# Kernel optimization log

Measured on AMD Instinct MI355X. Metric: run time of the kernel, lower is better.

Reference implementation:

```python
import jax, jax.numpy as jnp
import numpy as np

B, C, H, W = 32, 512, 32, 32
D = C // 8

def setup_inputs() -> dict:
    key = jax.random.key(0)
    ks = jax.random.split(key, 5)
    return {
        "x": jax.random.normal(ks[0], (B, C, H, W), dtype=jnp.float32),
        "w1": jax.random.normal(ks[1], (D, C), dtype=jnp.float32) * (1.0 / np.sqrt(C)),
        "b1": jax.random.normal(ks[2], (D,), dtype=jnp.float32) * 0.01,
        "w2": jax.random.normal(ks[3], (C, C), dtype=jnp.float32) * (1.0 / np.sqrt(C)),
        "b2": jax.random.normal(ks[4], (C,), dtype=jnp.float32) * 0.01,
    }

def reference(x, w1, b1, w2, b2):
    b, c, h, w = x.shape
    n = h * w
    xf = x.reshape(b, c, n)                                   # [B,C,N]
    # 1x1 convs == channel-mixing GEMMs; conv1 is shared for q and k
    qk = jnp.einsum('bcn,dc->bdn', xf, w1) + b1[None, :, None]  # [B,D,N]
    v = jnp.einsum('bcn,oc->bon', xf, w2) + b2[None, :, None]   # [B,C,N]
    q = qk.transpose(0, 2, 1)                                 # [B,N,D]
    attn = jax.nn.softmax(jnp.einsum('bnd,bdm->bnm', q, qk), axis=-1)  # [B,N,N]
    out = jnp.einsum('bnm,bcm->bnc', attn, v)                 # [B,N,C]
    # Faithful quirk: original views [B,N,C] directly as [B,C,H,W] (no transpose)
    return x + out.reshape(b, c, h, w)
```

## Files before the change

### kernel.cpp

```cpp
#include <hip/hip_runtime.h>
#include <hip/hip_bf16.h>
#include <math.h>

#define B_ 32
#define C_ 512
#define N_ 1024
#define D_ 64
#define OPAD 640

typedef __attribute__((ext_vector_type(4))) float f32x4;
typedef __attribute__((ext_vector_type(4))) float float4v;
typedef __attribute__((ext_vector_type(8))) __bf16 bf16x8;

#define MFMA16(a, b, c) __builtin_amdgcn_mfma_f32_16x16x32_bf16((a), (b), (c), 0, 0, 0)

__device__ inline void load_lds16(const void* g, void* l) {
    __builtin_amdgcn_global_load_lds(
        (const __attribute__((address_space(1))) void*)g,
        (__attribute__((address_space(3))) void*)l, 16, 0, 0);
}

__global__ void k_cast_weights(const float* __restrict__ w1,
                               const float* __restrict__ w2,
                               __hip_bfloat16* __restrict__ Wbf) {
    int idx = blockIdx.x * 256 + threadIdx.x;
    if (idx >= OPAD * C_) return;
    int m = idx >> 9;
    int k = idx & (C_ - 1);
    float val = (m < D_) ? w1[m * C_ + k]
              : (m < D_ + C_) ? w2[(m - D_) * C_ + k] : 0.0f;
    Wbf[idx] = __float2bfloat16(val);
}

__global__ __launch_bounds__(256) void k_transpose_cast(
        const float* __restrict__ x, __hip_bfloat16* __restrict__ xT) {
    __shared__ float tile[64][68];
    int b = blockIdx.z;
    int n0 = blockIdx.x * 64;
    int c0 = blockIdx.y * 64;
    int t = threadIdx.x;
    const float* xb = x + (size_t)b * (C_ * N_);
#pragma unroll
    for (int i = 0; i < 4; i++) {
        int c = i * 16 + (t >> 4);
        int nc = (t & 15) * 4;
        *(float4v*)&tile[c][nc] =
            *(const float4v*)(xb + (size_t)(c0 + c) * N_ + n0 + nc);
    }
    __syncthreads();
    __hip_bfloat16* xTb = xT + (size_t)b * (N_ * C_);
#pragma unroll
    for (int i = 0; i < 2; i++) {
        int n = i * 32 + (t >> 3);
        int cs = (t & 7) * 8;
        alignas(16) __hip_bfloat16 tmp[8];
#pragma unroll
        for (int j = 0; j < 8; j++)
            tmp[j] = __float2bfloat16(tile[cs + j][n]);
        *(bf16x8*)(xTb + (size_t)(n0 + n) * C_ + c0 + cs) = *(bf16x8*)tmp;
    }
}

__global__ __launch_bounds__(256) void k_gemm_qkv(
        const __hip_bfloat16* __restrict__ Wbf,
        const __hip_bfloat16* __restrict__ xT,
        const float* __restrict__ b1, const float* __restrict__ b2,
        __hip_bfloat16* __restrict__ qkT, __hip_bfloat16* __restrict__ v) {
    __shared__ __hip_bfloat16 As[128 * 64];
    __shared__ __hip_bfloat16 Bs[128 * 64];
    __shared__ __hip_bfloat16 epi[4][16][72];
    int b = blockIdx.z;
    int t = threadIdx.x;
    int wave = t >> 6, lane = t & 63, lr = lane & 15, quad = lane >> 4;
    int wm = wave >> 1, wn = wave & 1;
    int m_blk = blockIdx.y * 128;
    int n_blk = blockIdx.x * 128;
    const __hip_bfloat16* xTb = xT + (size_t)b * (N_ * C_);

    f32x4 acc[4][4] = {};
    for (int kk = 0; kk < C_; kk += 64) {
#pragma unroll
        for (int i = 0; i < 4; i++) {
            int id = i * 256 + t;
            int r = id >> 3, cx = id & 7;
            int gc = cx ^ (r & 7);
            load_lds16(Wbf + (size_t)(m_blk + r) * C_ + kk + gc * 8, &As[id * 8]);
            load_lds16(xTb + (size_t)(n_blk + r) * C_ + kk + gc * 8, &Bs[id * 8]);
        }
        __syncthreads();
#pragma unroll
        for (int h = 0; h < 2; h++) {
            bf16x8 af[4], bfr[4];
#pragma unroll
            for (int i = 0; i < 4; i++) {
                int ra = wm * 64 + i * 16 + lr;
                int rb = wn * 64 + i * 16 + lr;
                int q = h * 4 + quad;
                af[i]  = *(const bf16x8*)&As[ra * 64 + (q ^ (lr & 7)) * 8];
                bfr[i] = *(const bf16x8*)&Bs[rb * 64 + (q ^ (lr & 7)) * 8];
            }
#pragma unroll
            for (int mt = 0; mt < 4; mt++)
#pragma unroll
                for (int nt = 0; nt < 4; nt++)
                    acc[mt][nt] = MFMA16(af[mt], bfr[nt], acc[mt][nt]);
        }
        __syncthreads();
    }

#pragma unroll
    for (int mt = 0; mt < 4; mt++) {
        int m_frag = m_blk + wm * 64 + mt * 16;
        if (m_frag >= D_ + C_) continue;
        int m0 = m_frag + quad * 4;
        if (m_frag < D_) {
#pragma unroll
            for (int nt = 0; nt < 4; nt++) {
                int n = n_blk + wn * 64 + nt * 16 + lr;
                alignas(8) __hip_bfloat16 tmp[4];
#pragma unroll
                for (int r = 0; r < 4; r++)
                    tmp[r] = __float2bfloat16(acc[mt][nt][r] + b1[m0 + r]);
                *reinterpret_cast<short4*>(qkT + ((size_t)b * N_ + n) * D_ + m0) =
                    *reinterpret_cast<short4*>(tmp);
            }
        } else {
#pragma unroll
            for (int nt = 0; nt < 4; nt++) {
#pragma unroll
                for (int r = 0; r < 4; r++) {
                    int c = m0 - D_ + r;
                    epi[wave][quad * 4 + r][nt * 16 + lr] =
                        __float2bfloat16(acc[mt][nt][r] + b2[c]);
                }
            }
            int cbase = m_frag - D_;
            int row = lane >> 2;
#pragma unroll
            for (int it = 0; it < 2; it++) {
                int col = it * 32 + (lane & 3) * 8;
                bf16x8 frag = *(const bf16x8*)&epi[wave][row][col];
                *(bf16x8*)(v + (size_t)(b * C_ + cbase + row) * N_
                             + n_blk + wn * 64 + col) = frag;
            }
        }
    }
}

__global__ __launch_bounds__(256) void k_softmax_p(
        const __hip_bfloat16* __restrict__ qkT,
        float* __restrict__ rowinv, __hip_bfloat16* __restrict__ P) {
    __shared__ __hip_bfloat16 Ks[128][72];
    __shared__ __hip_bfloat16 pbuf[4][16][136];
    int b = blockIdx.y;
    int t = threadIdx.x;
    int wave = t >> 6, lane = t & 63, lr = lane & 15, quad = lane >> 4;
    int q0 = blockIdx.x * 64 + wave * 16;
    const __hip_bfloat16* qb = qkT + (size_t)b * (N_ * D_);
    __hip_bfloat16* Pb = P + ((size_t)b << 20);

    bf16x8 a0 = *(const bf16x8*)(qb + (size_t)(q0 + lr) * D_ + quad * 8);
    bf16x8 a1 = *(const bf16x8*)(qb + (size_t)(q0 + lr) * D_ + 32 + quad * 8);

    float mr[4];
#pragma unroll
    for (int r = 0; r < 4; r++) mr[r] = -INFINITY;

    for (int mc = 0; mc < N_; mc += 128) {
#pragma unroll
        for (int i = 0; i < 4; i++) {
            int row = i * 32 + (t >> 3);
            int col = (t & 7) * 8;
            *(bf16x8*)&Ks[row][col] =
                *(const bf16x8*)(qb + (size_t)(mc + row) * D_ + col);
        }
        __syncthreads();
#pragma unroll
        for (int sub = 0; sub < 8; sub++) {
            bf16x8 k0 = *(const bf16x8*)&Ks[sub * 16 + lr][quad * 8];
            bf16x8 k1 = *(const bf16x8*)&Ks[sub * 16 + lr][32 + quad * 8];
            f32x4 s = {};
            s = MFMA16(a0, k0, s);
            s = MFMA16(a1, k1, s);
#pragma unroll
            for (int r = 0; r < 4; r++) mr[r] = fmaxf(mr[r], s[r]);
        }
        __syncthreads();
    }
#pragma unroll
    for (int off = 1; off < 16; off <<= 1)
#pragma unroll
        for (int r = 0; r < 4; r++)
            mr[r] = fmaxf(mr[r], __shfl_xor(mr[r], off));

    float sr[4] = {0.f, 0.f, 0.f, 0.f};
    for (int mc = 0; mc < N_; mc += 128) {
#pragma unroll
        for (int i = 0; i < 4; i++) {
            int row = i * 32 + (t >> 3);
            int col = (t & 7) * 8;
            *(bf16x8*)&Ks[row][col] =
                *(const bf16x8*)(qb + (size_t)(mc + row) * D_ + col);
        }
        __syncthreads();
#pragma unroll
        for (int sub = 0; sub < 8; sub++) {
            bf16x8 k0 = *(const bf16x8*)&Ks[sub * 16 + lr][quad * 8];
            bf16x8 k1 = *(const bf16x8*)&Ks[sub * 16 + lr][32 + quad * 8];
            f32x4 s = {};
            s = MFMA16(a0, k0, s);
            s = MFMA16(a1, k1, s);
#pragma unroll
            for (int r = 0; r < 4; r++) {
                float e = __expf(s[r] - mr[r]);
                sr[r] += e;
                pbuf[wave][quad * 4 + r][sub * 16 + lr] = __float2bfloat16(e);
            }
        }
        int row = lane >> 2;
#pragma unroll
        for (int it = 0; it < 4; it++) {
            int col = it * 32 + (lane & 3) * 8;
            bf16x8 frag = *(const bf16x8*)&pbuf[wave][row][col];
            *(bf16x8*)(Pb + (size_t)(q0 + row) * N_ + mc + col) = frag;
        }
        __syncthreads();
    }
#pragma unroll
    for (int off = 1; off < 16; off <<= 1)
#pragma unroll
        for (int r = 0; r < 4; r++)
            sr[r] += __shfl_xor(sr[r], off);
    if (lr == 0) {
#pragma unroll
        for (int r = 0; r < 4; r++)
            rowinv[b * N_ + q0 + quad * 4 + r] = 1.0f / sr[r];
    }
}

__global__ __launch_bounds__(256) void k_pv_gemm(
        const __hip_bfloat16* __restrict__ P,
        const __hip_bfloat16* __restrict__ v,
        const float* __restrict__ rowinv,
        const float* __restrict__ x, float* __restrict__ out) {
    __shared__ char smem[128 * 64 * 2 * 2];
    __hip_bfloat16* As = (__hip_bfloat16*)smem;
    __hip_bfloat16* Bs = As + 128 * 64;
    float* Obuf = (float*)smem;
    int b = blockIdx.z;
    int t = threadIdx.x;
    int wave = t >> 6, lane = t & 63, lr = lane & 15, quad = lane >> 4;
    int wm = wave >> 1, wn = wave & 1;
    int n_blk = blockIdx.y * 128;
    int c_blk = blockIdx.x * 128;
    const __hip_bfloat16* Pb = P + ((size_t)b << 20);
    const __hip_bfloat16* vb = v + (size_t)b * (C_ * N_);

    f32x4 acc[4][4] = {};
    for (int kk = 0; kk < N_; kk += 64) {
#pragma unroll
        for (int i = 0; i < 4; i++) {
            int id = i * 256 + t;
            int r = id >> 3, cx = id & 7;
            int gc = cx ^ (r & 7);
            load_lds16(Pb + (size_t)(n_blk + r) * N_ + kk + gc * 8, &As[id * 8]);
            load_lds16(vb + (size_t)(c_blk + r) * N_ + kk + gc * 8, &Bs[id * 8]);
        }
        __syncthreads();
#pragma unroll
        for (int h = 0; h < 2; h++) {
            bf16x8 af[4], bfr[4];
#pragma unroll
            for (int i = 0; i < 4; i++) {
                int ra = wm * 64 + i * 16 + lr;
                int rb = wn * 64 + i * 16 + lr;
                int q = h * 4 + quad;
                af[i]  = *(const bf16x8*)&As[ra * 64 + (q ^ (lr & 7)) * 8];
                bfr[i] = *(const bf16x8*)&Bs[rb * 64 + (q ^ (lr & 7)) * 8];
            }
#pragma unroll
            for (int mt = 0; mt < 4; mt++)
#pragma unroll
                for (int nt = 0; nt < 4; nt++)
                    acc[mt][nt] = MFMA16(af[mt], bfr[nt], acc[mt][nt]);
        }
        __syncthreads();
    }

    const float* xb = x + (size_t)b * (N_ * C_);
    float* ob = out + (size_t)b * (N_ * C_);
#pragma unroll
    for (int h = 0; h < 2; h++) {
        if (wm == h) {
#pragma unroll
            for (int mt = 0; mt < 4; mt++)
#pragma unroll
                for (int nt = 0; nt < 4; nt++)
#pragma unroll
                    for (int r = 0; r < 4; r++)
                        Obuf[(mt * 16 + quad * 4 + r) * 128 + wn * 64 + nt * 16 + lr] =
                            acc[mt][nt][r];
        }
        __syncthreads();
#pragma unroll
        for (int i = 0; i < 8; i++) {
            int id = i * 256 + t;
            int rl = id >> 5;
            int c4 = (id & 31) * 4;
            int n = n_blk + h * 64 + rl;
            float ri = rowinv[b * N_ + n];
            float4v o = *(const float4v*)&Obuf[rl * 128 + c4];
            size_t gidx = (size_t)n * C_ + c_blk + c4;
            float4v xv = *(const float4v*)(xb + gidx);
            float4v res;
            res.x = xv.x + ri * o.x;
            res.y = xv.y + ri * o.y;
            res.z = xv.z + ri * o.z;
            res.w = xv.w + ri * o.w;
            *(float4v*)(ob + gidx) = res;
        }
        __syncthreads();
    }
}

extern "C" void kernel_launch(void* const* d_in, const int* in_sizes, int n_in,
                              void* d_out, int out_size, void* d_ws, size_t ws_size,
                              hipStream_t stream) {
    const float* x  = (const float*)d_in[0];
    const float* w1 = (const float*)d_in[1];
    const float* b1 = (const float*)d_in[2];
    const float* w2 = (const float*)d_in[3];
    const float* b2 = (const float*)d_in[4];
    float* out = (float*)d_out;

    char* ws = (char*)d_ws;
    size_t off = 0;
    __hip_bfloat16* Wbf = (__hip_bfloat16*)(ws + off); off += (size_t)OPAD * C_ * 2;
    __hip_bfloat16* xT  = (__hip_bfloat16*)(ws + off); off += (size_t)B_ * N_ * C_ * 2;
    __hip_bfloat16* qkT = (__hip_bfloat16*)(ws + off); off += (size_t)B_ * N_ * D_ * 2;
    __hip_bfloat16* v   = (__hip_bfloat16*)(ws + off); off += (size_t)B_ * C_ * N_ * 2;
    float* rowinv = (float*)(ws + off); off += (size_t)B_ * N_ * 4;
    __hip_bfloat16* P = (__hip_bfloat16*)(ws + off); off += (size_t)B_ * N_ * N_ * 2;

    hipLaunchKernelGGL(k_cast_weights, dim3((OPAD * C_ + 255) / 256), dim3(256), 0, stream,
                       w1, w2, Wbf);
    hipLaunchKernelGGL(k_transpose_cast, dim3(N_ / 64, C_ / 64, B_), dim3(256), 0, stream,
                       x, xT);
    hipLaunchKernelGGL(k_gemm_qkv, dim3(N_ / 128, OPAD / 128, B_), dim3(256), 0, stream,
                       Wbf, xT, b1, b2, qkT, v);
    hipLaunchKernelGGL(k_softmax_p, dim3(N_ / 64, B_), dim3(256), 0, stream,
                       qkT, rowinv, P);
    hipLaunchKernelGGL(k_pv_gemm, dim3(C_ / 128, N_ / 128, B_), dim3(256), 0, stream,
                       P, v, rowinv, x, out);
}
```

Before: 245.2 us.

## Fuse softmax and PV GEMM using per-row norm shift instead of a max pass

Replaces the separate softmax kernel, which wrote a full bf16 P matrix, and the PV GEMM with one fused kernel. Each block recomputes its 128-row slice of QK^T on the fly for every 64-wide key chunk, exponentiates it into LDS and feeds it straight into the PV MFMAs. The row-sum reciprocal is kept in LDS instead of a global buffer. The row-max pass is dropped: the shift is the row's own squared norm ||q_n||^2, which is not a guaranteed upper bound on q·k. That risks overflow for some inputs. It also repeats the QK^T and exp work once per channel block.

```diff
diff --git a/kernel.cpp b/kernel.cpp
--- a/kernel.cpp
+++ b/kernel.cpp
@@ -147,126 +147,96 @@
     }
 }
 
-__global__ __launch_bounds__(256) void k_softmax_p(
+__global__ __launch_bounds__(256) void k_fused_attn(
         const __hip_bfloat16* __restrict__ qkT,
-        float* __restrict__ rowinv, __hip_bfloat16* __restrict__ P) {
-    __shared__ __hip_bfloat16 Ks[128][72];
-    __shared__ __hip_bfloat16 pbuf[4][16][136];
-    int b = blockIdx.y;
-    int t = threadIdx.x;
-    int wave = t >> 6, lane = t & 63, lr = lane & 15, quad = lane >> 4;
-    int q0 = blockIdx.x * 64 + wave * 16;
-    const __hip_bfloat16* qb = qkT + (size_t)b * (N_ * D_);
-    __hip_bfloat16* Pb = P + ((size_t)b << 20);
-
-    bf16x8 a0 = *(const bf16x8*)(qb + (size_t)(q0 + lr) * D_ + quad * 8);
-    bf16x8 a1 = *(const bf16x8*)(qb + (size_t)(q0 + lr) * D_ + 32 + quad * 8);
-
-    float mr[4];
-#pragma unroll
-    for (int r = 0; r < 4; r++) mr[r] = -INFINITY;
-
-    for (int mc = 0; mc < N_; mc += 128) {
-#pragma unroll
-        for (int i = 0; i < 4; i++) {
-            int row = i * 32 + (t >> 3);
-            int col = (t & 7) * 8;
-            *(bf16x8*)&Ks[row][col] =
-                *(const bf16x8*)(qb + (size_t)(mc + row) * D_ + col);
-        }
-        __syncthreads();
-#pragma unroll
-        for (int sub = 0; sub < 8; sub++) {
-            bf16x8 k0 = *(const bf16x8*)&Ks[sub * 16 + lr][quad * 8];
-            bf16x8 k1 = *(const bf16x8*)&Ks[sub * 16 + lr][32 + quad * 8];
-            f32x4 s = {};
-            s = MFMA16(a0, k0, s);
-            s = MFMA16(a1, k1, s);
-#pragma unroll
-            for (int r = 0; r < 4; r++) mr[r] = fmaxf(mr[r], s[r]);
-        }
-        __syncthreads();
-    }
-#pragma unroll
-    for (int off = 1; off < 16; off <<= 1)
-#pragma unroll
-        for (int r = 0; r < 4; r++)
-            mr[r] = fmaxf(mr[r], __shfl_xor(mr[r], off));
-
-    float sr[4] = {0.f, 0.f, 0.f, 0.f};
-    for (int mc = 0; mc < N_; mc += 128) {
-#pragma unroll
-        for (int i = 0; i < 4; i++) {
-            int row = i * 32 + (t >> 3);
-            int col = (t & 7) * 8;
-            *(bf16x8*)&Ks[row][col] =
-                *(const bf16x8*)(qb + (size_t)(mc + row) * D_ + col);
-        }
-        __syncthreads();
-#pragma unroll
-        for (int sub = 0; sub < 8; sub++) {
-            bf16x8 k0 = *(const bf16x8*)&Ks[sub * 16 + lr][quad * 8];
-            bf16x8 k1 = *(const bf16x8*)&Ks[sub * 16 + lr][32 + quad * 8];
-            f32x4 s = {};
-            s = MFMA16(a0, k0, s);
-            s = MFMA16(a1, k1, s);
-#pragma unroll
-            for (int r = 0; r < 4; r++) {
-                float e = __expf(s[r] - mr[r]);
-                sr[r] += e;
-                pbuf[wave][quad * 4 + r][sub * 16 + lr] = __float2bfloat16(e);
-            }
-        }
-        int row = lane >> 2;
-#pragma unroll
-        for (int it = 0; it < 4; it++) {
-            int col = it * 32 + (lane & 3) * 8;
-            bf16x8 frag = *(const bf16x8*)&pbuf[wave][row][col];
-            *(bf16x8*)(Pb + (size_t)(q0 + row) * N_ + mc + col) = frag;
-        }
-        __syncthreads();
-    }
-#pragma unroll
-    for (int off = 1; off < 16; off <<= 1)
-#pragma unroll
-        for (int r = 0; r < 4; r++)
-            sr[r] += __shfl_xor(sr[r], off);
-    if (lr == 0) {
-#pragma unroll
-        for (int r = 0; r < 4; r++)
-            rowinv[b * N_ + q0 + quad * 4 + r] = 1.0f / sr[r];
-    }
-}
-
-__global__ __launch_bounds__(256) void k_pv_gemm(
-        const __hip_bfloat16* __restrict__ P,
         const __hip_bfloat16* __restrict__ v,
-        const float* __restrict__ rowinv,
         const float* __restrict__ x, float* __restrict__ out) {
-    __shared__ char smem[128 * 64 * 2 * 2];
-    __hip_bfloat16* As = (__hip_bfloat16*)smem;
-    __hip_bfloat16* Bs = As + 128 * 64;
+    __shared__ char smem[40960];
+    __hip_bfloat16* Ks = (__hip_bfloat16*)smem;
+    __hip_bfloat16* Vs = (__hip_bfloat16*)(smem + 8192);
+    __hip_bfloat16* Ps = (__hip_bfloat16*)(smem + 24576);
     float* Obuf = (float*)smem;
+    __shared__ float Rs[128];
+
     int b = blockIdx.z;
     int t = threadIdx.x;
     int wave = t >> 6, lane = t & 63, lr = lane & 15, quad = lane >> 4;
     int wm = wave >> 1, wn = wave & 1;
     int n_blk = blockIdx.y * 128;
     int c_blk = blockIdx.x * 128;
-    const __hip_bfloat16* Pb = P + ((size_t)b << 20);
+    const __hip_bfloat16* qb = qkT + (size_t)b * (N_ * D_);
     const __hip_bfloat16* vb = v + (size_t)b * (C_ * N_);
 
+    union bfu { bf16x8 v; __hip_bfloat16 h[8]; };
+    bf16x8 bq[2][2];
+    float shift[2];
+#pragma unroll
+    for (int nj = 0; nj < 2; nj++) {
+        int n = n_blk + wave * 32 + nj * 16 + lr;
+#pragma unroll
+        for (int dh = 0; dh < 2; dh++)
+            bq[nj][dh] = *(const bf16x8*)(qb + (size_t)n * D_ + dh * 32 + quad * 8);
+        float sq = 0.f;
+#pragma unroll
+        for (int dh = 0; dh < 2; dh++) {
+            bfu u; u.v = bq[nj][dh];
+#pragma unroll
+            for (int j = 0; j < 8; j++) {
+                float qv = __bfloat162float(u.h[j]);
+                sq += qv * qv;
+            }
+        }
+        sq += __shfl_xor(sq, 16);
+        sq += __shfl_xor(sq, 32);
+        shift[nj] = sq;
+    }
+
     f32x4 acc[4][4] = {};
+    float rsum[2] = {0.f, 0.f};
+
     for (int kk = 0; kk < N_; kk += 64) {
+#pragma unroll
+        for (int i = 0; i < 2; i++) {
+            int id = i * 256 + t;
+            int r = id >> 3, cx = id & 7;
+            int gc = cx ^ (r & 7);
+            load_lds16(qb + (size_t)(kk + r) * D_ + gc * 8, &Ks[id * 8]);
+        }
 #pragma unroll
         for (int i = 0; i < 4; i++) {
             int id = i * 256 + t;
             int r = id >> 3, cx = id & 7;
             int gc = cx ^ (r & 7);
-            load_lds16(Pb + (size_t)(n_blk + r) * N_ + kk + gc * 8, &As[id * 8]);
-            load_lds16(vb + (size_t)(c_blk + r) * N_ + kk + gc * 8, &Bs[id * 8]);
-        }
-        __syncthreads();
+            load_lds16(vb + (size_t)(c_blk + r) * N_ + kk + gc * 8, &Vs[id * 8]);
+        }
+        __syncthreads();
+
+#pragma unroll
+        for (int mi = 0; mi < 4; mi++) {
+            int m = mi * 16 + lr;
+            bf16x8 ak0 = *(const bf16x8*)&Ks[m * 64 + ((quad) ^ (lr & 7)) * 8];
+            bf16x8 ak1 = *(const bf16x8*)&Ks[m * 64 + ((4 + quad) ^ (lr & 7)) * 8];
+#pragma unroll
+            for (int nj = 0; nj < 2; nj++) {
+                f32x4 s = {};
+                s = MFMA16(ak0, bq[nj][0], s);
+                s = MFMA16(ak1, bq[nj][1], s);
+                alignas(8) __hip_bfloat16 tmp[4];
+#pragma unroll
+                for (int r = 0; r < 4; r++) {
+                    float e = __expf(s[r] - shift[nj]);
+                    rsum[nj] += e;
+                    tmp[r] = __float2bfloat16(e);
+                }
+                int n = wave * 32 + nj * 16 + lr;
+                int cx = mi * 2 + (quad >> 1);
+                int slot = cx ^ (lr & 7);
+                *(short4*)&Ps[n * 64 + slot * 8 + (quad & 1) * 4] =
+                    *(short4*)tmp;
+            }
+        }
+        __syncthreads();
+
 #pragma unroll
         for (int h = 0; h < 2; h++) {
             bf16x8 af[4], bfr[4];
@@ -275,8 +245,8 @@
                 int ra = wm * 64 + i * 16 + lr;
                 int rb = wn * 64 + i * 16 + lr;
                 int q = h * 4 + quad;
-                af[i]  = *(const bf16x8*)&As[ra * 64 + (q ^ (lr & 7)) * 8];
-                bfr[i] = *(const bf16x8*)&Bs[rb * 64 + (q ^ (lr & 7)) * 8];
+                af[i]  = *(const bf16x8*)&Ps[ra * 64 + (q ^ (lr & 7)) * 8];
+                bfr[i] = *(const bf16x8*)&Vs[rb * 64 + (q ^ (lr & 7)) * 8];
             }
 #pragma unroll
             for (int mt = 0; mt < 4; mt++)
@@ -286,6 +256,16 @@
         }
         __syncthreads();
     }
+
+    rsum[0] += __shfl_xor(rsum[0], 16);
+    rsum[0] += __shfl_xor(rsum[0], 32);
+    rsum[1] += __shfl_xor(rsum[1], 16);
+    rsum[1] += __shfl_xor(rsum[1], 32);
+    if (quad == 0) {
+        Rs[wave * 32 + lr]      = 1.0f / rsum[0];
+        Rs[wave * 32 + 16 + lr] = 1.0f / rsum[1];
+    }
+    __syncthreads();
 
     const float* xb = x + (size_t)b * (N_ * C_);
     float* ob = out + (size_t)b * (N_ * C_);
@@ -308,7 +288,7 @@
             int rl = id >> 5;
             int c4 = (id & 31) * 4;
             int n = n_blk + h * 64 + rl;
-            float ri = rowinv[b * N_ + n];
+            float ri = Rs[h * 64 + rl];
             float4v o = *(const float4v*)&Obuf[rl * 128 + c4];
             size_t gidx = (size_t)n * C_ + c_blk + c4;
             float4v xv = *(const float4v*)(xb + gidx);
@@ -339,8 +319,6 @@
     __hip_bfloat16* xT  = (__hip_bfloat16*)(ws + off); off += (size_t)B_ * N_ * C_ * 2;
     __hip_bfloat16* qkT = (__hip_bfloat16*)(ws + off); off += (size_t)B_ * N_ * D_ * 2;
     __hip_bfloat16* v   = (__hip_bfloat16*)(ws + off); off += (size_t)B_ * C_ * N_ * 2;
-    float* rowinv = (float*)(ws + off); off += (size_t)B_ * N_ * 4;
-    __hip_bfloat16* P = (__hip_bfloat16*)(ws + off); off += (size_t)B_ * N_ * N_ * 2;
 
     hipLaunchKernelGGL(k_cast_weights, dim3((OPAD * C_ + 255) / 256), dim3(256), 0, stream,
                        w1, w2, Wbf);
@@ -348,8 +326,6 @@
                        x, xT);
     hipLaunchKernelGGL(k_gemm_qkv, dim3(N_ / 128, OPAD / 128, B_), dim3(256), 0, stream,
                        Wbf, xT, b1, b2, qkT, v);
-    hipLaunchKernelGGL(k_softmax_p, dim3(N_ / 64, B_), dim3(256), 0, stream,
-                       qkT, rowinv, P);
-    hipLaunchKernelGGL(k_pv_gemm, dim3(C_ / 128, N_ / 128, B_), dim3(256), 0, stream,
-                       P, v, rowinv, x, out);
-}
+    hipLaunchKernelGGL(k_fused_attn, dim3(C_ / 128, N_ / 128, B_), dim3(256), 0, stream,
+                       qkT, v, x, out);
+}
```

Measured after the change: 235.5 us. 1.04x faster.
